# Optimization experiments

Measured on AMD Instinct MI355X. Metric: run time of the kernel, lower is better.

## Reference

```python
import jax, jax.numpy as jnp
import numpy as np

N_MASTER = 100000
N_BOND = 200000
N_GLOB = 5000
E1 = 400000
E2 = 100000
D_IN = 64
D_OUT = 64
H = 4
SLOPE = 0.2  # leaky relu negative slope


def _mlp(x, W0, b0, W1, b1, W2):
    # LinearN with num_fc_layers=3: ELU, ELU, Identity (last layer no bias)
    h = jax.nn.elu(x @ W0 + b0)
    h = jax.nn.elu(h @ W1 + b1)
    return h @ W2  # (N, H*D_OUT)


def setup_inputs() -> dict:
    key = jax.random.key(0)
    ks = jax.random.split(key, 32)
    s = 0.1  # weight scale
    d = {
        "master_feats": jax.random.normal(ks[0], (N_MASTER, D_IN), jnp.float32),
        "bond_feats": jax.random.normal(ks[1], (N_BOND, D_IN), jnp.float32),
        "global_feats": jax.random.normal(ks[2], (N_GLOB, D_IN), jnp.float32),
        "atom_W0": jax.random.normal(ks[3], (D_IN, D_OUT), jnp.float32) * s,
        "atom_b0": jnp.zeros((D_OUT,), jnp.float32),
        "atom_W1": jax.random.normal(ks[4], (D_OUT, D_OUT), jnp.float32) * s,
        "atom_b1": jnp.zeros((D_OUT,), jnp.float32),
        "atom_W2": jax.random.normal(ks[5], (D_OUT, H * D_OUT), jnp.float32) * s,
        "bond_W0": jax.random.normal(ks[6], (D_IN, D_OUT), jnp.float32) * s,
        "bond_b0": jnp.zeros((D_OUT,), jnp.float32),
        "bond_W1": jax.random.normal(ks[7], (D_OUT, D_OUT), jnp.float32) * s,
        "bond_b1": jnp.zeros((D_OUT,), jnp.float32),
        "bond_W2": jax.random.normal(ks[8], (D_OUT, H * D_OUT), jnp.float32) * s,
        "glob_W0": jax.random.normal(ks[9], (D_IN, D_OUT), jnp.float32) * s,
        "glob_b0": jnp.zeros((D_OUT,), jnp.float32),
        "glob_W1": jax.random.normal(ks[10], (D_OUT, D_OUT), jnp.float32) * s,
        "glob_b1": jnp.zeros((D_OUT,), jnp.float32),
        "glob_W2": jax.random.normal(ks[11], (D_OUT, H * D_OUT), jnp.float32) * s,
        "attn_l": jax.random.normal(ks[12], (H, D_OUT), jnp.float32) * s,
        "attn_r": jax.random.normal(ks[13], (H, D_OUT), jnp.float32) * s,
        "e1_src": jax.random.randint(ks[14], (E1,), 0, N_BOND, jnp.int32),
        "e1_dst": jax.random.randint(ks[15], (E1,), 0, N_MASTER, jnp.int32),
        "e2_src": jax.random.randint(ks[16], (E2,), 0, N_GLOB, jnp.int32),
        "e2_dst": jax.random.randint(ks[17], (E2,), 0, N_MASTER, jnp.int32),
    }
    return d


def reference(master_feats, bond_feats, global_feats,
              atom_W0, atom_b0, atom_W1, atom_b1, atom_W2,
              bond_W0, bond_b0, bond_W1, bond_b1, bond_W2,
              glob_W0, glob_b0, glob_W1, glob_b1, glob_W2,
              attn_l, attn_r, e1_src, e1_dst, e2_src, e2_dst):
    # Per-node-type projections to (N, H, D_OUT)
    ft_m = _mlp(master_feats, atom_W0, atom_b0, atom_W1, atom_b1, atom_W2).reshape(N_MASTER, H, D_OUT)
    ft_b = _mlp(bond_feats, bond_W0, bond_b0, bond_W1, bond_b1, bond_W2).reshape(N_BOND, H, D_OUT)
    ft_g = _mlp(global_feats, glob_W0, glob_b0, glob_W1, glob_b1, glob_W2).reshape(N_GLOB, H, D_OUT)

    er = jnp.einsum('nhd,hd->nh', ft_m, attn_r)  # master (dst) scores
    el_b = jnp.einsum('nhd,hd->nh', ft_b, attn_l)
    el_g = jnp.einsum('nhd,hd->nh', ft_g, attn_l)

    # Per-edge logits: u_add_v then leaky relu
    e1 = jax.nn.leaky_relu(el_b[e1_src] + er[e1_dst], negative_slope=SLOPE)  # (E1, H)
    e2 = jax.nn.leaky_relu(el_g[e2_src] + er[e2_dst], negative_slope=SLOPE)  # (E2, H)

    # Joint edge softmax over all incoming edges per master node
    dst_all = jnp.concatenate([e1_dst, e2_dst])  # (E1+E2,)
    e_all = jnp.concatenate([e1, e2], axis=0)    # (E1+E2, H)
    emax = jax.ops.segment_max(e_all, dst_all, num_segments=N_MASTER)  # (N, H)
    ex = jnp.exp(e_all - emax[dst_all])
    esum = jax.ops.segment_sum(ex, dst_all, num_segments=N_MASTER)     # (N, H)
    a = ex / esum[dst_all]                                             # (E, H)

    # Aggregate: u_mul_e, sum per destination master node
    src_ft = jnp.concatenate([ft_b[e1_src], ft_g[e2_src]], axis=0)     # (E, H, D)
    msgs = src_ft * a[:, :, None]
    rst = jax.ops.segment_sum(msgs, dst_all, num_segments=N_MASTER)    # (N, H, D)
    return rst
```

## Files before the change

### kernel.cpp

```cpp
#include <hip/hip_runtime.h>

#define NM 100000
#define NB 200000
#define NG 5000
#define NE1 400000
#define NE2 100000
#define NE (NE1 + NE2)
#define NMP 100004
#define SCAN_BLOCKS 391

typedef __attribute__((ext_vector_type(8))) short bf16x8;
typedef __attribute__((ext_vector_type(4))) short short4v;
typedef __attribute__((ext_vector_type(4))) float f32x4;

__device__ __forceinline__ unsigned short f2bf(float f) {
    unsigned int u = __float_as_uint(f);
    u += 0x7FFFu + ((u >> 16) & 1u);
    return (unsigned short)(u >> 16);
}
__device__ __forceinline__ float bf2f(unsigned short u) {
    return __uint_as_float((unsigned int)u << 16);
}
__device__ __forceinline__ float elu_f(float x) {
    return x > 0.f ? x : __expf(x) - 1.f;
}
__device__ __forceinline__ char* swz(char* base, int j, int byteoff) {
    return base + j * 128 + ((((byteoff >> 4) ^ (j & 7)) << 4) | (byteoff & 15));
}

struct WEnt { const float* W; short* o; int I; int off; };
struct WAll { WEnt e[9]; };

__global__ __launch_bounds__(256) void wprep_all_kernel(WAll a)
{
    const int idx = blockIdx.x * 256 + threadIdx.x;
    #pragma unroll
    for (int j = 8; j >= 0; --j) {
        if (idx >= a.e[j].off) {
            const int local = idx - a.e[j].off;
            const int I = a.e[j].I;
            const int i = local >> 6, k = local & 63;
            a.e[j].o[local] = (short)f2bf(a.e[j].W[k * I + i]);
            break;
        }
    }
}

__global__ __launch_bounds__(256) void mlp_mfma_kernel(
    const float* __restrict__ x, int N,
    const short* __restrict__ W0t, const float* __restrict__ b0,
    const short* __restrict__ W1t, const float* __restrict__ b1,
    const short* __restrict__ W2t,
    const float* __restrict__ attn,
    float* __restrict__ score,
    unsigned short* __restrict__ ft_out)
{
    __shared__ __attribute__((aligned(128))) char ldsA[64 * 128];
    __shared__ __attribute__((aligned(128))) char ldsB[64 * 128];

    const int tid = threadIdx.x;
    const int w = tid >> 6, l = tid & 63;
    const int g = l >> 4, c = l & 15;
    const int r0 = blockIdx.x << 6;

    {
        const int j = tid >> 2, q = tid & 3;
        const int row = r0 + j;
        bf16x8 o0 = (bf16x8)0, o1 = (bf16x8)0;
        if (row < N) {
            const float4* xp = (const float4*)(x + ((size_t)row << 6) + (q << 4));
            #pragma unroll
            for (int u = 0; u < 2; ++u) {
                float4 v = xp[u];
                o0[u*4+0] = (short)f2bf(v.x); o0[u*4+1] = (short)f2bf(v.y);
                o0[u*4+2] = (short)f2bf(v.z); o0[u*4+3] = (short)f2bf(v.w);
            }
            #pragma unroll
            for (int u = 0; u < 2; ++u) {
                float4 v = xp[u + 2];
                o1[u*4+0] = (short)f2bf(v.x); o1[u*4+1] = (short)f2bf(v.y);
                o1[u*4+2] = (short)f2bf(v.z); o1[u*4+3] = (short)f2bf(v.w);
            }
        }
        *(bf16x8*)swz(ldsA, j, q * 32)      = o0;
        *(bf16x8*)swz(ldsA, j, q * 32 + 16) = o1;
    }
    __syncthreads();

    char* src = ldsA;
    char* dst = ldsB;
    #pragma unroll
    for (int layer = 0; layer < 2; ++layer) {
        const short* Wt = layer ? W1t : W0t;
        const float* bb = layer ? b1 : b0;
        f32x4 acc[4] = {};
        #pragma unroll
        for (int step = 0; step < 2; ++step) {
            bf16x8 a = *(const bf16x8*)(Wt + (((16 * w + c) << 6) + 32 * step + 8 * g));
            #pragma unroll
            for (int t = 0; t < 4; ++t) {
                const int j = 16 * t + c;
                bf16x8 b = *(const bf16x8*)swz(src, j, 64 * step + 16 * g);
                acc[t] = __builtin_amdgcn_mfma_f32_16x16x32_bf16(a, b, acc[t], 0, 0, 0);
            }
        }
        const int i0 = 16 * w + 4 * g;
        const float4 bias = *(const float4*)(bb + i0);
        #pragma unroll
        for (int t = 0; t < 4; ++t) {
            const int j = 16 * t + c;
            short4v o;
            o[0] = (short)f2bf(elu_f(acc[t][0] + bias.x));
            o[1] = (short)f2bf(elu_f(acc[t][1] + bias.y));
            o[2] = (short)f2bf(elu_f(acc[t][2] + bias.z));
            o[3] = (short)f2bf(elu_f(acc[t][3] + bias.w));
            *(short4v*)swz(dst, j, 32 * w + 8 * g) = o;
        }
        __syncthreads();
        char* tmp = src; src = dst; dst = tmp;
    }

    {
        f32x4 acc[4][4] = {};
        #pragma unroll
        for (int step = 0; step < 2; ++step) {
            bf16x8 bfr[4];
            #pragma unroll
            for (int t = 0; t < 4; ++t)
                bfr[t] = *(const bf16x8*)swz(src, 16 * t + c, 64 * step + 16 * g);
            #pragma unroll
            for (int it = 0; it < 4; ++it) {
                bf16x8 a = *(const bf16x8*)(W2t + (((64 * w + 16 * it + c) << 6) + 32 * step + 8 * g));
                #pragma unroll
                for (int t = 0; t < 4; ++t)
                    acc[it][t] = __builtin_amdgcn_mfma_f32_16x16x32_bf16(a, bfr[t], acc[it][t], 0, 0, 0);
            }
        }
        float4 av[4];
        #pragma unroll
        for (int it = 0; it < 4; ++it)
            av[it] = *(const float4*)(attn + 64 * w + 16 * it + 4 * g);

        #pragma unroll
        for (int t = 0; t < 4; ++t) {
            const int row = r0 + 16 * t + c;
            float p = 0.f;
            #pragma unroll
            for (int it = 0; it < 4; ++it) {
                p += acc[it][t][0] * av[it].x + acc[it][t][1] * av[it].y
                   + acc[it][t][2] * av[it].z + acc[it][t][3] * av[it].w;
            }
            p += __shfl_xor(p, 16);
            p += __shfl_xor(p, 32);
            if (row < N) {
                if (g == 0) score[(row << 2) + w] = p;
                if (ft_out) {
                    #pragma unroll
                    for (int it = 0; it < 4; ++it) {
                        short4v o;
                        o[0] = (short)f2bf(acc[it][t][0]);
                        o[1] = (short)f2bf(acc[it][t][1]);
                        o[2] = (short)f2bf(acc[it][t][2]);
                        o[3] = (short)f2bf(acc[it][t][3]);
                        __builtin_nontemporal_store(o,
                            (short4v*)(ft_out + ((size_t)row << 8) + 64 * w + 16 * it + 4 * g));
                    }
                }
            }
        }
    }
}

__global__ void hist_kernel(const int* __restrict__ e1_dst,
                            const int* __restrict__ e2_dst,
                            int* __restrict__ counts)
{
    int i = blockIdx.x * blockDim.x + threadIdx.x;
    if (i < NE1) atomicAdd(&counts[e1_dst[i]], 1);
    else if (i < NE) atomicAdd(&counts[e2_dst[i - NE1]], 1);
}

__global__ __launch_bounds__(256) void scan1_kernel(
    const int* __restrict__ counts,
    int* __restrict__ prefix_inc,
    int* __restrict__ blocksums)
{
    const int i = blockIdx.x * 256 + threadIdx.x;
    const int lane = threadIdx.x & 63, wv = threadIdx.x >> 6;
    int v = (i < NM) ? counts[i] : 0;
    int x = v;
    #pragma unroll
    for (int o = 1; o < 64; o <<= 1) {
        int u = __shfl_up(x, o);
        if (lane >= o) x += u;
    }
    __shared__ int wsum[4];
    if (lane == 63) wsum[wv] = x;
    __syncthreads();
    int add = 0;
    #pragma unroll
    for (int k = 0; k < 3; ++k) add += (k < wv) ? wsum[k] : 0;
    x += add;
    if (i < NM) prefix_inc[i] = x;
    if (threadIdx.x == 255) blocksums[blockIdx.x] = x;
}

__global__ __launch_bounds__(512) void scan2_kernel(int* __restrict__ blocksums)
{
    const int t = threadIdx.x;
    const int lane = t & 63, wv = t >> 6;
    int v = (t < SCAN_BLOCKS) ? blocksums[t] : 0;
    int x = v;
    #pragma unroll
    for (int o = 1; o < 64; o <<= 1) {
        int u = __shfl_up(x, o);
        if (lane >= o) x += u;
    }
    __shared__ int wsum[8];
    if (lane == 63) wsum[wv] = x;
    __syncthreads();
    int add = 0;
    #pragma unroll
    for (int k = 0; k < 7; ++k) add += (k < wv) ? wsum[k] : 0;
    x += add;
    if (t < SCAN_BLOCKS) blocksums[t] = x - v;
}

__global__ __launch_bounds__(256) void scan3_kernel(
    const int* __restrict__ counts,
    const int* __restrict__ prefix_inc,
    const int* __restrict__ blocksums,
    int* __restrict__ offsets,
    int* __restrict__ cursor)
{
    const int i = blockIdx.x * 256 + threadIdx.x;
    if (i > NM) return;
    if (i == NM) { offsets[NM] = NE; return; }
    const int off = prefix_inc[i] - counts[i] + blocksums[blockIdx.x];
    offsets[i] = off;
    cursor[i]  = off;
}

__global__ void fill_kernel(const int* __restrict__ e1_src,
                            const int* __restrict__ e1_dst,
                            const int* __restrict__ e2_src,
                            const int* __restrict__ e2_dst,
                            const float* __restrict__ er,
                            const float* __restrict__ el_b,
                            const float* __restrict__ el_g,
                            int* __restrict__ cursor,
                            int* __restrict__ rows,
                            float4* __restrict__ vsort)
{
    int i = blockIdx.x * blockDim.x + threadIdx.x;
    if (i >= NE) return;
    int dst, src, row;
    const float* el;
    if (i < NE1) { src = e1_src[i]; dst = e1_dst[i]; row = src;      el = el_b; }
    else { int j = i - NE1; src = e2_src[j]; dst = e2_dst[j]; row = NB + src; el = el_g; }
    const float4 l4 = *(const float4*)(el + (src << 2));
    const float4 r4 = *(const float4*)(er + (dst << 2));
    float4 v;
    v.x = l4.x + r4.x; v.x = v.x > 0.f ? v.x : 0.2f * v.x;
    v.y = l4.y + r4.y; v.y = v.y > 0.f ? v.y : 0.2f * v.y;
    v.z = l4.z + r4.z; v.z = v.z > 0.f ? v.z : 0.2f * v.z;
    v.w = l4.w + r4.w; v.w = v.w > 0.f ? v.w : 0.2f * v.w;
    int p = atomicAdd(&cursor[dst], 1);
    rows[p] = row;
    vsort[p] = v;
}

__global__ __launch_bounds__(256) void aggregate_kernel(
    const int* __restrict__ offsets,
    const int* __restrict__ rows,
    const float* __restrict__ vsort,
    const unsigned short* __restrict__ ft,
    float* __restrict__ out)
{
    const int w = threadIdx.x >> 6, l = threadIdx.x & 63;
    const int h   = l >> 4;
    const int e16 = l & 15;
    const int f4  = l << 2;

    const int n = (blockIdx.x << 2) + w;
    if (n >= NM) return;

    const int start = offsets[n];
    const int deg   = offsets[n + 1] - start;

    f32x4 o = {};
    float s = 0.f;
    for (int b = 0; b < deg; b += 16) {
        const int rem = min(deg - b, 16);
        int   row_l = 0;
        float v_l   = 0.f;
        if (e16 < rem) {
            row_l = rows[start + b + e16];
            v_l   = vsort[((start + b + e16) << 2) + h];
        }
        short4v ftv[16];
        #pragma unroll
        for (int e = 0; e < 16; ++e) {
            if (e < rem) {
                const int row = __shfl(row_l, e);
                ftv[e] = *(const short4v*)(ft + ((size_t)row << 8) + f4);
            }
        }
        #pragma unroll
        for (int e = 0; e < 16; ++e) {
            if (e < rem) {
                const float wgt = __expf(__shfl(v_l, (h << 4) + e));
                s += wgt;
                o[0] = fmaf(bf2f((unsigned short)ftv[e][0]), wgt, o[0]);
                o[1] = fmaf(bf2f((unsigned short)ftv[e][1]), wgt, o[1]);
                o[2] = fmaf(bf2f((unsigned short)ftv[e][2]), wgt, o[2]);
                o[3] = fmaf(bf2f((unsigned short)ftv[e][3]), wgt, o[3]);
            }
        }
    }
    if (deg > 0) {
        const float inv = 1.f / s;
        o[0] *= inv; o[1] *= inv; o[2] *= inv; o[3] *= inv;
    }
    __builtin_nontemporal_store(o, (f32x4*)(out + ((size_t)n << 8) + f4));
}

extern "C" void kernel_launch(void* const* d_in, const int* in_sizes, int n_in,
                              void* d_out, int out_size, void* d_ws, size_t ws_size,
                              hipStream_t stream)
{
    const float* master = (const float*)d_in[0];
    const float* bond   = (const float*)d_in[1];
    const float* glob   = (const float*)d_in[2];
    const float* aW0 = (const float*)d_in[3];
    const float* ab0 = (const float*)d_in[4];
    const float* aW1 = (const float*)d_in[5];
    const float* ab1 = (const float*)d_in[6];
    const float* aW2 = (const float*)d_in[7];
    const float* bW0 = (const float*)d_in[8];
    const float* bb0 = (const float*)d_in[9];
    const float* bW1 = (const float*)d_in[10];
    const float* bb1 = (const float*)d_in[11];
    const float* bW2 = (const float*)d_in[12];
    const float* gW0 = (const float*)d_in[13];
    const float* gb0 = (const float*)d_in[14];
    const float* gW1 = (const float*)d_in[15];
    const float* gb1 = (const float*)d_in[16];
    const float* gW2 = (const float*)d_in[17];
    const float* attn_l = (const float*)d_in[18];
    const float* attn_r = (const float*)d_in[19];
    const int* e1_src = (const int*)d_in[20];
    const int* e1_dst = (const int*)d_in[21];
    const int* e2_src = (const int*)d_in[22];
    const int* e2_dst = (const int*)d_in[23];
    float* out = (float*)d_out;

    float* ws   = (float*)d_ws;
    unsigned short* ft_b = (unsigned short*)ws;
    unsigned short* ft_g = ft_b + (size_t)NB * 256;
    float* er   = (float*)(ft_g + (size_t)NG * 256);
    float* el_b = er + (size_t)NM * 4;
    float* el_g = el_b + (size_t)NB * 4;
    int* counts  = (int*)(el_g + (size_t)NG * 4);
    int* offsets = counts + NMP;
    int* cursor  = offsets + NMP;
    int* rows    = cursor + NMP;
    float4* vsort = (float4*)(rows + NE);
    int* prefix_inc = (int*)(vsort + NE);
    int* blocksums  = prefix_inc + NMP;
    short* wtA = (short*)(blocksums + 512);
    short* wtB = wtA + 24576;
    short* wtG = wtB + 24576;

    hipMemsetAsync(counts, 0, sizeof(int) * NM, stream);

    WAll wa;
    wa.e[0] = {aW0, wtA,          64,     0};
    wa.e[1] = {aW1, wtA + 4096,   64,  4096};
    wa.e[2] = {aW2, wtA + 8192,  256,  8192};
    wa.e[3] = {bW0, wtB,          64, 24576};
    wa.e[4] = {bW1, wtB + 4096,   64, 28672};
    wa.e[5] = {bW2, wtB + 8192,  256, 32768};
    wa.e[6] = {gW0, wtG,          64, 49152};
    wa.e[7] = {gW1, wtG + 4096,   64, 53248};
    wa.e[8] = {gW2, wtG + 8192,  256, 57344};
    wprep_all_kernel<<<288, 256, 0, stream>>>(wa);

    mlp_mfma_kernel<<<(NM + 63) / 64, 256, 0, stream>>>(
        master, NM, wtA, ab0, wtA + 4096, ab1, wtA + 8192, attn_r, er, nullptr);
    mlp_mfma_kernel<<<(NB + 63) / 64, 256, 0, stream>>>(
        bond, NB, wtB, bb0, wtB + 4096, bb1, wtB + 8192, attn_l, el_b, ft_b);
    mlp_mfma_kernel<<<(NG + 63) / 64, 256, 0, stream>>>(
        glob, NG, wtG, gb0, wtG + 4096, gb1, wtG + 8192, attn_l, el_g, ft_g);

    hist_kernel<<<(NE + 255) / 256, 256, 0, stream>>>(e1_dst, e2_dst, counts);
    scan1_kernel<<<SCAN_BLOCKS, 256, 0, stream>>>(counts, prefix_inc, blocksums);
    scan2_kernel<<<1, 512, 0, stream>>>(blocksums);
    scan3_kernel<<<SCAN_BLOCKS + 1, 256, 0, stream>>>(counts, prefix_inc, blocksums,
                                                      offsets, cursor);
    fill_kernel<<<(NE + 255) / 256, 256, 0, stream>>>(e1_src, e1_dst, e2_src, e2_dst,
                                                      er, el_b, el_g,
                                                      cursor, rows, vsort);
    aggregate_kernel<<<(NM + 3) / 4, 256, 0, stream>>>(offsets, rows,
                                                       (const float*)vsort,
                                                       ft_b, out);
}
```

Measured before the change: 223.2 us.

## Defer last MLP layer until after aggregation and fold attention into precomputed vectors

Since the final layer is linear with no bias, the per-edge weighted sum of ft can be computed as the weighted sum of the 64-wide hidden h2, followed by a single W2 matmul per destination node. Bond and glob contributions are kept in separate accumulators because they use different W2 matrices. Attention scores are computed as h2 dot (W2·attn), precomputed per head by a small kernel. This cuts the gathered feature width from 256 to 64 bf16 per edge and removes the W2 MFMA from the MLP kernels. In exchange the aggregate kernel gains an LDS stage and an MFMA epilogue, and the normalized aggregate is rounded to bf16 before the final matmul.

```diff
diff --git a/kernel.cpp b/kernel.cpp
--- a/kernel.cpp
+++ b/kernel.cpp
@@ -29,13 +29,13 @@
 }
 
 struct WEnt { const float* W; short* o; int I; int off; };
-struct WAll { WEnt e[9]; };
+struct WAll { WEnt e[6]; };
 
 __global__ __launch_bounds__(256) void wprep_all_kernel(WAll a)
 {
     const int idx = blockIdx.x * 256 + threadIdx.x;
     #pragma unroll
-    for (int j = 8; j >= 0; --j) {
+    for (int j = 5; j >= 0; --j) {
         if (idx >= a.e[j].off) {
             const int local = idx - a.e[j].off;
             const int I = a.e[j].I;
@@ -46,14 +46,37 @@
     }
 }
 
-__global__ __launch_bounds__(256) void mlp_mfma_kernel(
+__global__ __launch_bounds__(256) void wt2prep_kernel(
+    const float* __restrict__ W2b, const float* __restrict__ W2g,
+    short* __restrict__ wt2)
+{
+    const int idx = blockIdx.x * 256 + threadIdx.x;
+    const int i = idx >> 7, k = idx & 127;
+    const float v = (k < 64) ? W2b[(k << 8) + i] : W2g[((k - 64) << 8) + i];
+    wt2[idx] = (short)f2bf(v);
+}
+
+__global__ __launch_bounds__(256) void eff_kernel(
+    const float* __restrict__ W2, const float* __restrict__ attn,
+    float* __restrict__ eff)
+{
+    const int t = threadIdx.x;
+    const int h = t >> 6, k = t & 63;
+    const float* wrow = W2 + (k << 8) + (h << 6);
+    const float* arow = attn + (h << 6);
+    float s = 0.f;
+    #pragma unroll 8
+    for (int d = 0; d < 64; ++d) s = fmaf(wrow[d], arow[d], s);
+    eff[(h << 6) + k] = s;
+}
+
+__global__ __launch_bounds__(256, 4) void mlp2_kernel(
     const float* __restrict__ x, int N,
     const short* __restrict__ W0t, const float* __restrict__ b0,
     const short* __restrict__ W1t, const float* __restrict__ b1,
-    const short* __restrict__ W2t,
-    const float* __restrict__ attn,
+    const float* __restrict__ eff,
     float* __restrict__ score,
-    unsigned short* __restrict__ ft_out)
+    unsigned short* __restrict__ h2_out)
 {
     __shared__ __attribute__((aligned(128))) char ldsA[64 * 128];
     __shared__ __attribute__((aligned(128))) char ldsB[64 * 128];
@@ -121,52 +144,31 @@
     }
 
     {
-        f32x4 acc[4][4] = {};
+        const int j = tid >> 2, h = tid & 3;
+        const int row = r0 + j;
+        float s = 0.f;
         #pragma unroll
-        for (int step = 0; step < 2; ++step) {
-            bf16x8 bfr[4];
-            #pragma unroll
-            for (int t = 0; t < 4; ++t)
-                bfr[t] = *(const bf16x8*)swz(src, 16 * t + c, 64 * step + 16 * g);
-            #pragma unroll
-            for (int it = 0; it < 4; ++it) {
-                bf16x8 a = *(const bf16x8*)(W2t + (((64 * w + 16 * it + c) << 6) + 32 * step + 8 * g));
-                #pragma unroll
-                for (int t = 0; t < 4; ++t)
-                    acc[it][t] = __builtin_amdgcn_mfma_f32_16x16x32_bf16(a, bfr[t], acc[it][t], 0, 0, 0);
-            }
-        }
-        float4 av[4];
-        #pragma unroll
-        for (int it = 0; it < 4; ++it)
-            av[it] = *(const float4*)(attn + 64 * w + 16 * it + 4 * g);
-
-        #pragma unroll
-        for (int t = 0; t < 4; ++t) {
-            const int row = r0 + 16 * t + c;
-            float p = 0.f;
-            #pragma unroll
-            for (int it = 0; it < 4; ++it) {
-                p += acc[it][t][0] * av[it].x + acc[it][t][1] * av[it].y
-                   + acc[it][t][2] * av[it].z + acc[it][t][3] * av[it].w;
-            }
-            p += __shfl_xor(p, 16);
-            p += __shfl_xor(p, 32);
-            if (row < N) {
-                if (g == 0) score[(row << 2) + w] = p;
-                if (ft_out) {
-                    #pragma unroll
-                    for (int it = 0; it < 4; ++it) {
-                        short4v o;
-                        o[0] = (short)f2bf(acc[it][t][0]);
-                        o[1] = (short)f2bf(acc[it][t][1]);
-                        o[2] = (short)f2bf(acc[it][t][2]);
-                        o[3] = (short)f2bf(acc[it][t][3]);
-                        __builtin_nontemporal_store(o,
-                            (short4v*)(ft_out + ((size_t)row << 8) + 64 * w + 16 * it + 4 * g));
-                    }
-                }
-            }
+        for (int c8 = 0; c8 < 8; ++c8) {
+            bf16x8 v = *(const bf16x8*)swz(src, j, c8 * 16);
+            const float4 e0 = *(const float4*)(eff + (h << 6) + (c8 << 3));
+            const float4 e1 = *(const float4*)(eff + (h << 6) + (c8 << 3) + 4);
+            s += bf2f((unsigned short)v[0]) * e0.x + bf2f((unsigned short)v[1]) * e0.y
+               + bf2f((unsigned short)v[2]) * e0.z + bf2f((unsigned short)v[3]) * e0.w
+               + bf2f((unsigned short)v[4]) * e1.x + bf2f((unsigned short)v[5]) * e1.y
+               + bf2f((unsigned short)v[6]) * e1.z + bf2f((unsigned short)v[7]) * e1.w;
+        }
+        if (row < N) score[(row << 2) + h] = s;
+    }
+
+    if (h2_out) {
+        const int j = tid >> 2, q = tid & 3;
+        const int row = r0 + j;
+        if (row < N) {
+            bf16x8 v0 = *(const bf16x8*)swz(src, j, q * 32);
+            bf16x8 v1 = *(const bf16x8*)swz(src, j, q * 32 + 16);
+            unsigned short* p = h2_out + ((size_t)row << 6) + (q << 4);
+            *(bf16x8*)p       = v0;
+            *(bf16x8*)(p + 8) = v1;
         }
     }
 }
@@ -270,59 +272,98 @@
     vsort[p] = v;
 }
 
-__global__ __launch_bounds__(256) void aggregate_kernel(
+#define AGSTR 304
+__global__ __launch_bounds__(256) void aggregate_fused_kernel(
     const int* __restrict__ offsets,
     const int* __restrict__ rows,
     const float* __restrict__ vsort,
-    const unsigned short* __restrict__ ft,
+    const unsigned short* __restrict__ h2,
+    const short* __restrict__ wt2,
     float* __restrict__ out)
 {
+    __shared__ __attribute__((aligned(16))) char agg_lds[16 * 4 * AGSTR];
+
     const int w = threadIdx.x >> 6, l = threadIdx.x & 63;
-    const int h   = l >> 4;
+    const int h = l >> 4;
+    const int c = l & 15;
     const int e16 = l & 15;
-    const int f4  = l << 2;
-
-    const int n = (blockIdx.x << 2) + w;
-    if (n >= NM) return;
-
-    const int start = offsets[n];
-    const int deg   = offsets[n + 1] - start;
-
-    f32x4 o = {};
-    float s = 0.f;
-    for (int b = 0; b < deg; b += 16) {
-        const int rem = min(deg - b, 16);
-        int   row_l = 0;
-        float v_l   = 0.f;
-        if (e16 < rem) {
-            row_l = rows[start + b + e16];
-            v_l   = vsort[((start + b + e16) << 2) + h];
-        }
-        short4v ftv[16];
+    const int n0 = blockIdx.x << 4;
+
+    #pragma unroll
+    for (int j = 0; j < 4; ++j) {
+        const int n = n0 + 4 * w + j;
+        const int start = offsets[n];
+        const int deg   = offsets[n + 1] - start;
+
+        f32x4 acc = {}, accg = {};
+        float s = 0.f;
+        for (int b = 0; b < deg; b += 16) {
+            const int rem = min(deg - b, 16);
+            int   row_l = 0;
+            float v_l   = 0.f;
+            if (e16 < rem) {
+                row_l = rows[start + b + e16];
+                v_l   = vsort[((start + b + e16) << 2) + h];
+            }
+            int rws[16];
+            short4v gv[16];
+            #pragma unroll
+            for (int e = 0; e < 16; ++e) {
+                if (e < rem) {
+                    rws[e] = __shfl(row_l, e);
+                    gv[e] = *(const short4v*)(h2 + ((size_t)rws[e] << 6) + (c << 2));
+                }
+            }
+            #pragma unroll
+            for (int e = 0; e < 16; ++e) {
+                if (e < rem) {
+                    const float wgt = __expf(__shfl(v_l, (h << 4) + e));
+                    s += wgt;
+                    const f32x4 fv = {bf2f((unsigned short)gv[e][0]),
+                                      bf2f((unsigned short)gv[e][1]),
+                                      bf2f((unsigned short)gv[e][2]),
+                                      bf2f((unsigned short)gv[e][3])};
+                    if (rws[e] >= NB) {
+                        accg[0] = fmaf(fv[0], wgt, accg[0]);
+                        accg[1] = fmaf(fv[1], wgt, accg[1]);
+                        accg[2] = fmaf(fv[2], wgt, accg[2]);
+                        accg[3] = fmaf(fv[3], wgt, accg[3]);
+                    } else {
+                        acc[0] = fmaf(fv[0], wgt, acc[0]);
+                        acc[1] = fmaf(fv[1], wgt, acc[1]);
+                        acc[2] = fmaf(fv[2], wgt, acc[2]);
+                        acc[3] = fmaf(fv[3], wgt, acc[3]);
+                    }
+                }
+            }
+        }
+        const float inv = (deg > 0) ? 1.f / s : 0.f;
+        char* p = agg_lds + ((4 * w + j) * 4 + h) * AGSTR;
+        short4v ob, og;
+        ob[0] = (short)f2bf(acc[0] * inv);  ob[1] = (short)f2bf(acc[1] * inv);
+        ob[2] = (short)f2bf(acc[2] * inv);  ob[3] = (short)f2bf(acc[3] * inv);
+        og[0] = (short)f2bf(accg[0] * inv); og[1] = (short)f2bf(accg[1] * inv);
+        og[2] = (short)f2bf(accg[2] * inv); og[3] = (short)f2bf(accg[3] * inv);
+        *(short4v*)(p + 8 * c)       = ob;
+        *(short4v*)(p + 128 + 8 * c) = og;
+    }
+    __syncthreads();
+
+    {
+        const int g = l >> 4;
+        float* outrow = out + ((size_t)(n0 + c) << 8) + (w << 6);
         #pragma unroll
-        for (int e = 0; e < 16; ++e) {
-            if (e < rem) {
-                const int row = __shfl(row_l, e);
-                ftv[e] = *(const short4v*)(ft + ((size_t)row << 8) + f4);
-            }
-        }
-        #pragma unroll
-        for (int e = 0; e < 16; ++e) {
-            if (e < rem) {
-                const float wgt = __expf(__shfl(v_l, (h << 4) + e));
-                s += wgt;
-                o[0] = fmaf(bf2f((unsigned short)ftv[e][0]), wgt, o[0]);
-                o[1] = fmaf(bf2f((unsigned short)ftv[e][1]), wgt, o[1]);
-                o[2] = fmaf(bf2f((unsigned short)ftv[e][2]), wgt, o[2]);
-                o[3] = fmaf(bf2f((unsigned short)ftv[e][3]), wgt, o[3]);
-            }
-        }
-    }
-    if (deg > 0) {
-        const float inv = 1.f / s;
-        o[0] *= inv; o[1] *= inv; o[2] *= inv; o[3] *= inv;
-    }
-    __builtin_nontemporal_store(o, (f32x4*)(out + ((size_t)n << 8) + f4));
+        for (int it = 0; it < 4; ++it) {
+            f32x4 oacc = {};
+            #pragma unroll
+            for (int st = 0; st < 4; ++st) {
+                bf16x8 a = *(const bf16x8*)(wt2 + (((64 * w + 16 * it + c) << 7) + 32 * st + 8 * g));
+                bf16x8 bfrag = *(const bf16x8*)(agg_lds + (c * 4 + w) * AGSTR + 64 * st + 16 * g);
+                oacc = __builtin_amdgcn_mfma_f32_16x16x32_bf16(a, bfrag, oacc, 0, 0, 0);
+            }
+            *(f32x4*)(outrow + 16 * it + 4 * g) = oacc;
+        }
+    }
 }
 
 extern "C" void kernel_launch(void* const* d_in, const int* in_sizes, int n_in,
@@ -355,10 +396,8 @@
     const int* e2_dst = (const int*)d_in[23];
     float* out = (float*)d_out;
 
-    float* ws   = (float*)d_ws;
-    unsigned short* ft_b = (unsigned short*)ws;
-    unsigned short* ft_g = ft_b + (size_t)NB * 256;
-    float* er   = (float*)(ft_g + (size_t)NG * 256);
+    unsigned short* h2 = (unsigned short*)d_ws;
+    float* er   = (float*)(h2 + (size_t)(NB + NG) * 64);
     float* el_b = er + (size_t)NM * 4;
     float* el_g = el_b + (size_t)NB * 4;
     int* counts  = (int*)(el_g + (size_t)NG * 4);
@@ -368,30 +407,35 @@
     float4* vsort = (float4*)(rows + NE);
     int* prefix_inc = (int*)(vsort + NE);
     int* blocksums  = prefix_inc + NMP;
-    short* wtA = (short*)(blocksums + 512);
-    short* wtB = wtA + 24576;
-    short* wtG = wtB + 24576;
+    float* effR  = (float*)(blocksums + 512);
+    float* effLB = effR + 256;
+    float* effLG = effLB + 256;
+    short* wt2 = (short*)(effLG + 256);
+    short* wtA = wt2 + 32768;
+    short* wtB = wtA + 8192;
+    short* wtG = wtB + 8192;
 
     hipMemsetAsync(counts, 0, sizeof(int) * NM, stream);
 
     WAll wa;
-    wa.e[0] = {aW0, wtA,          64,     0};
-    wa.e[1] = {aW1, wtA + 4096,   64,  4096};
-    wa.e[2] = {aW2, wtA + 8192,  256,  8192};
-    wa.e[3] = {bW0, wtB,          64, 24576};
-    wa.e[4] = {bW1, wtB + 4096,   64, 28672};
-    wa.e[5] = {bW2, wtB + 8192,  256, 32768};
-    wa.e[6] = {gW0, wtG,          64, 49152};
-    wa.e[7] = {gW1, wtG + 4096,   64, 53248};
-    wa.e[8] = {gW2, wtG + 8192,  256, 57344};
-    wprep_all_kernel<<<288, 256, 0, stream>>>(wa);
-
-    mlp_mfma_kernel<<<(NM + 63) / 64, 256, 0, stream>>>(
-        master, NM, wtA, ab0, wtA + 4096, ab1, wtA + 8192, attn_r, er, nullptr);
-    mlp_mfma_kernel<<<(NB + 63) / 64, 256, 0, stream>>>(
-        bond, NB, wtB, bb0, wtB + 4096, bb1, wtB + 8192, attn_l, el_b, ft_b);
-    mlp_mfma_kernel<<<(NG + 63) / 64, 256, 0, stream>>>(
-        glob, NG, wtG, gb0, wtG + 4096, gb1, wtG + 8192, attn_l, el_g, ft_g);
+    wa.e[0] = {aW0, wtA,         64,     0};
+    wa.e[1] = {aW1, wtA + 4096,  64,  4096};
+    wa.e[2] = {bW0, wtB,         64,  8192};
+    wa.e[3] = {bW1, wtB + 4096,  64, 12288};
+    wa.e[4] = {gW0, wtG,         64, 16384};
+    wa.e[5] = {gW1, wtG + 4096,  64, 20480};
+    wprep_all_kernel<<<96, 256, 0, stream>>>(wa);
+    wt2prep_kernel<<<128, 256, 0, stream>>>(bW2, gW2, wt2);
+    eff_kernel<<<1, 256, 0, stream>>>(aW2, attn_r, effR);
+    eff_kernel<<<1, 256, 0, stream>>>(bW2, attn_l, effLB);
+    eff_kernel<<<1, 256, 0, stream>>>(gW2, attn_l, effLG);
+
+    mlp2_kernel<<<(NM + 63) / 64, 256, 0, stream>>>(
+        master, NM, wtA, ab0, wtA + 4096, ab1, effR, er, nullptr);
+    mlp2_kernel<<<(NB + 63) / 64, 256, 0, stream>>>(
+        bond, NB, wtB, bb0, wtB + 4096, bb1, effLB, el_b, h2);
+    mlp2_kernel<<<(NG + 63) / 64, 256, 0, stream>>>(
+        glob, NG, wtG, gb0, wtG + 4096, gb1, effLG, el_g, h2 + (size_t)NB * 64);
 
     hist_kernel<<<(NE + 255) / 256, 256, 0, stream>>>(e1_dst, e2_dst, counts);
     scan1_kernel<<<SCAN_BLOCKS, 256, 0, stream>>>(counts, prefix_inc, blocksums);
@@ -401,7 +445,7 @@
     fill_kernel<<<(NE + 255) / 256, 256, 0, stream>>>(e1_src, e1_dst, e2_src, e2_dst,
                                                       er, el_b, el_g,
                                                       cursor, rows, vsort);
-    aggregate_kernel<<<(NM + 3) / 4, 256, 0, stream>>>(offsets, rows,
-                                                       (const float*)vsort,
-                                                       ft_b, out);
-}
+    aggregate_fused_kernel<<<NM / 16, 256, 0, stream>>>(offsets, rows,
+                                                        (const float*)vsort,
+                                                        h2, wt2, out);
+}
```

Result: slower. 259.0 us (+16.1%).
